# Kernel tuning notes

Measured on AMD Instinct MI355X. Metric: run time of the kernel, lower is better.

The kernel has to match this reference:

```python
import jax, jax.numpy as jnp
import numpy as np

NUM_HEADS = 4
GROUPS = 8          # min(8, ch) with ch=256
EPS = 1e-5          # torch GroupNorm default eps


def setup_inputs() -> dict:
    key = jax.random.key(0)
    ks = jax.random.split(key, 3)
    b, c, h, w = 8, 256, 32, 32
    x = jax.random.normal(ks[0], (b, c, h, w), jnp.float32)
    gn_gamma = jnp.ones((c,), jnp.float32)
    gn_beta = jnp.zeros((c,), jnp.float32)
    qkv_w = jax.random.normal(ks[1], (3 * c, c), jnp.float32) * (c ** -0.5)
    qkv_b = jnp.zeros((3 * c,), jnp.float32)
    proj_w = jax.random.normal(ks[2], (c, c), jnp.float32) * (c ** -0.5)
    proj_b = jnp.zeros((c,), jnp.float32)
    return {"x": x, "gn_gamma": gn_gamma, "gn_beta": gn_beta,
            "qkv_w": qkv_w, "qkv_b": qkv_b, "proj_w": proj_w, "proj_b": proj_b}


def _group_norm(x, gamma, beta):
    b, c, h, w = x.shape
    xg = x.reshape(b, GROUPS, c // GROUPS, h, w)
    mean = xg.mean(axis=(2, 3, 4), keepdims=True)
    var = xg.var(axis=(2, 3, 4), keepdims=True)
    xn = ((xg - mean) * jax.lax.rsqrt(var + EPS)).reshape(b, c, h, w)
    return xn * gamma[None, :, None, None] + beta[None, :, None, None]


def reference(x, gn_gamma, gn_beta, qkv_w, qkv_b, proj_w, proj_b):
    b, c, h, w = x.shape
    dh = c // NUM_HEADS
    xn = _group_norm(x, gn_gamma, gn_beta)
    # 1x1 conv == channel matmul
    qkv = jnp.einsum('oc,bchw->bohw', qkv_w, xn) + qkv_b[None, :, None, None]
    qkv = qkv.reshape(b, 3, NUM_HEADS, dh, h * w)
    q, k, v = qkv[:, 0], qkv[:, 1], qkv[:, 2]   # each (b, n, dh, hw)
    scale = dh ** -0.5
    # full (hw x hw) attention matrix, matching the original explicit einsum
    attn = jax.nn.softmax(jnp.einsum('bncd,bnce->bnde', q, k) * scale, axis=-1)
    out = jnp.einsum('bnde,bnce->bncd', attn, v).reshape(b, c, h, w)
    out = jnp.einsum('oc,bchw->bohw', proj_w, out) + proj_b[None, :, None, None]
    return x + out
```

## Files before the change

### kernel.cpp

```cpp
#include <hip/hip_runtime.h>
#include <stdint.h>

typedef __attribute__((ext_vector_type(8))) short short8;
typedef __attribute__((ext_vector_type(4))) float f32x4;

#define BB 8
#define CC 256
#define PP 1024
#define NH 4
#define DH 64

__device__ __forceinline__ unsigned short f2bf(float f) {
  union { float f; unsigned u; } v; v.f = f;
  unsigned r = v.u + 0x7FFFu + ((v.u >> 16) & 1u);
  return (unsigned short)(r >> 16);
}

__device__ __forceinline__ f32x4 mfma16(short8 a, short8 b, f32x4 c) {
  return __builtin_amdgcn_mfma_f32_16x16x32_bf16(a, b, c, 0, 0, 0);
}

__global__ __launch_bounds__(256) void prep(
    const float* __restrict__ x, float2* __restrict__ part,
    const float* __restrict__ qkvw, const float* __restrict__ projw,
    unsigned short* __restrict__ wall) {
  int blk = blockIdx.x;
  int tid = threadIdx.x;
  if (blk < 512) {
    int sl = blk & 7, g = (blk >> 3) & 7, b = blk >> 6;
    const float4* xb =
        (const float4*)(x + (size_t)(b * CC + g * 32) * PP) + sl * 1024;
    float s = 0.f, q = 0.f;
    for (int i = tid; i < 1024; i += 256) {
      float4 v = xb[i];
      s += v.x + v.y + v.z + v.w;
      q += v.x * v.x + v.y * v.y + v.z * v.z + v.w * v.w;
    }
    for (int off = 32; off > 0; off >>= 1) {
      s += __shfl_down(s, off);
      q += __shfl_down(q, off);
    }
    __shared__ float rs[4], rq[4];
    int w = tid >> 6;
    if ((tid & 63) == 0) { rs[w] = s; rq[w] = q; }
    __syncthreads();
    if (tid == 0)
      part[blk] = make_float2(rs[0] + rs[1] + rs[2] + rs[3],
                              rq[0] + rq[1] + rq[2] + rq[3]);
  } else {
    int i4 = (blk - 512) * 256 + tid;
    float4 v = (i4 < 49152) ? ((const float4*)qkvw)[i4]
                            : ((const float4*)projw)[i4 - 49152];
    ushort4 o;
    o.x = f2bf(v.x); o.y = f2bf(v.y); o.z = f2bf(v.z); o.w = f2bf(v.w);
    ((ushort4*)wall)[i4] = o;
  }
}

__global__ __launch_bounds__(256) void norm_t(
    const float* __restrict__ x, const float2* __restrict__ part,
    const float* __restrict__ gamma, const float* __restrict__ beta,
    unsigned short* __restrict__ xnT) {
  int p0 = blockIdx.x * 64, c0 = blockIdx.y * 64, b = blockIdx.z;
  int tid = threadIdx.x;
  __shared__ float ms[2], rstd[2];
  __shared__ unsigned short T[64][72];
  if (tid < 2) {
    int g = blockIdx.y * 2 + tid;
    float S = 0.f, Q = 0.f;
    for (int i = 0; i < 8; ++i) {
      float2 pp = part[b * 64 + g * 8 + i];
      S += pp.x; Q += pp.y;
    }
    float mean = S * (1.f / 32768.f);
    float var = Q * (1.f / 32768.f) - mean * mean;
    ms[tid] = mean;
    rstd[tid] = rsqrtf(var + 1e-5f);
  }
  __syncthreads();
  for (int it = 0; it < 4; ++it) {
    int l = tid + 256 * it;
    int cc = l >> 4, p4 = l & 15;
    int c = c0 + cc, gi = cc >> 5;
    float sc = rstd[gi] * gamma[c];
    float sh = beta[c] - ms[gi] * sc;
    float4 v = *(const float4*)(x + (size_t)(b * CC + c) * PP + p0 + p4 * 4);
    T[p4 * 4 + 0][cc] = f2bf(v.x * sc + sh);
    T[p4 * 4 + 1][cc] = f2bf(v.y * sc + sh);
    T[p4 * 4 + 2][cc] = f2bf(v.z * sc + sh);
    T[p4 * 4 + 3][cc] = f2bf(v.w * sc + sh);
  }
  __syncthreads();
  for (int it = 0; it < 2; ++it) {
    int l = tid + 256 * it;
    int p = l >> 3, seg = l & 7;
    *(short8*)(xnT + ((size_t)b * PP + p0 + p) * CC + c0 + seg * 8) =
        *(const short8*)&T[p][seg * 8];
  }
}

__global__ __launch_bounds__(256) void qkv_gemm(
    const unsigned short* __restrict__ xnT, const unsigned short* __restrict__ wbf,
    const float* __restrict__ qkvb, unsigned short* __restrict__ qb,
    unsigned short* __restrict__ kb, unsigned short* __restrict__ vT) {
  int p0 = blockIdx.x * 128, o0 = blockIdx.y * 128, b = blockIdx.z;
  int tid = threadIdx.x;
  int w = tid >> 6, lane = tid & 63, lq = lane >> 4, ln = lane & 15;
  int wy = w >> 1, wx = w & 1;
  __shared__ unsigned short A_l[128][40];
  __shared__ unsigned short B_l[128][40];
  f32x4 acc[4][4];
  for (int i = 0; i < 4; ++i)
    for (int j = 0; j < 4; ++j) acc[i][j] = (f32x4){0.f, 0.f, 0.f, 0.f};
  for (int kc = 0; kc < 256; kc += 32) {
    for (int it = 0; it < 2; ++it) {
      int l = tid + 256 * it;
      int row = l >> 2, seg = l & 3;
      *(short8*)&A_l[row][seg * 8] =
          *(const short8*)(xnT + ((size_t)b * PP + p0 + row) * CC + kc + seg * 8);
      *(short8*)&B_l[row][seg * 8] =
          *(const short8*)(wbf + (size_t)(o0 + row) * CC + kc + seg * 8);
    }
    __syncthreads();
    short8 af[4], bf[4];
    for (int i = 0; i < 4; ++i)
      af[i] = *(const short8*)&A_l[wy * 64 + i * 16 + ln][lq * 8];
    for (int j = 0; j < 4; ++j)
      bf[j] = *(const short8*)&B_l[wx * 64 + j * 16 + ln][lq * 8];
    for (int i = 0; i < 4; ++i)
      for (int j = 0; j < 4; ++j) acc[i][j] = mfma16(af[i], bf[j], acc[i][j]);
    __syncthreads();
  }
  for (int i = 0; i < 4; ++i) {
    for (int j = 0; j < 4; ++j) {
      int o = o0 + wx * 64 + j * 16 + ln;
      int s = o >> 8, h = (o >> 6) & 3, ch = o & 63;
      float bias = qkvb[o];
      float mul = (s == 0) ? 0.125f : 1.0f;
      size_t bh = (size_t)b * NH + h;
      for (int r = 0; r < 4; ++r) {
        int p = p0 + wy * 64 + i * 16 + lq * 4 + r;
        unsigned short val = f2bf((acc[i][j][r] + bias) * mul);
        if (s == 2) {
          vT[(bh * DH + ch) * PP + p] = val;
        } else {
          unsigned short* dst = (s == 0) ? qb : kb;
          dst[(bh * PP + p) * DH + ch] = val;
        }
      }
    }
  }
}

__global__ __launch_bounds__(256) void attn(
    const unsigned short* __restrict__ qb, const unsigned short* __restrict__ kb,
    const unsigned short* __restrict__ vT, unsigned short* __restrict__ attnT) {
  int d0 = blockIdx.x * 64, h = blockIdx.y, b = blockIdx.z;
  int tid = threadIdx.x;
  int w = tid >> 6, lane = tid & 63, lq = lane >> 4, ln = lane & 15;
  size_t bh = (size_t)b * NH + h;
  const unsigned short* qbase = qb + bh * PP * DH;
  const unsigned short* kbase = kb + bh * PP * DH;
  const unsigned short* vbase = vT + bh * DH * PP;
  __shared__ unsigned short K_l[128][72];
  __shared__ unsigned short V_l[64][136];
  __shared__ unsigned short P_l[64][140];
  unsigned short (*O_l)[72] = (unsigned short (*)[72]) & P_l[0][0];

  int ke = tid >> 1, kseg = tid & 1;
  int vch = tid >> 2, vseg = tid & 3;

  short8 qf[2];
  {
    int d = d0 + w * 16 + ln;
    qf[0] = *(const short8*)(qbase + (size_t)d * DH + lq * 8);
    qf[1] = *(const short8*)(qbase + (size_t)d * DH + 32 + lq * 8);
  }
  float l_sum = 0.f;
  f32x4 o_acc[4];
  for (int i = 0; i < 4; ++i) o_acc[i] = (f32x4){0.f, 0.f, 0.f, 0.f};

  short8 kr[4], vr[4];
#pragma unroll
  for (int i = 0; i < 4; ++i)
    kr[i] = *(const short8*)(kbase + (size_t)ke * DH + kseg * 32 + i * 8);
#pragma unroll
  for (int i = 0; i < 4; ++i)
    vr[i] = *(const short8*)(vbase + (size_t)vch * PP + vseg * 32 + i * 8);

  for (int e0 = 0; e0 < PP; e0 += 128) {
#pragma unroll
    for (int i = 0; i < 4; ++i)
      *(short8*)&K_l[ke][kseg * 32 + i * 8] = kr[i];
#pragma unroll
    for (int i = 0; i < 4; ++i)
      *(short8*)&V_l[vch][vseg * 32 + i * 8] = vr[i];
    if (e0 + 128 < PP) {
      int en = e0 + 128;
#pragma unroll
      for (int i = 0; i < 4; ++i)
        kr[i] = *(const short8*)(kbase + (size_t)(en + ke) * DH + kseg * 32 + i * 8);
#pragma unroll
      for (int i = 0; i < 4; ++i)
        vr[i] = *(const short8*)(vbase + (size_t)vch * PP + en + vseg * 32 + i * 8);
    }
    __syncthreads();
    f32x4 sc[8];
#pragma unroll
    for (int ns = 0; ns < 8; ++ns) {
      f32x4 a = (f32x4){0.f, 0.f, 0.f, 0.f};
      a = mfma16(*(const short8*)&K_l[ns * 16 + ln][lq * 8], qf[0], a);
      a = mfma16(*(const short8*)&K_l[ns * 16 + ln][32 + lq * 8], qf[1], a);
      sc[ns] = a;
    }
#pragma unroll
    for (int ns = 0; ns < 8; ++ns) {
      float p0 = __expf(fminf(sc[ns][0], 60.f));
      float p1 = __expf(fminf(sc[ns][1], 60.f));
      float p2 = __expf(fminf(sc[ns][2], 60.f));
      float p3 = __expf(fminf(sc[ns][3], 60.f));
      l_sum += (p0 + p1) + (p2 + p3);
      union { unsigned short u[4]; unsigned long long ll; } pk;
      pk.u[0] = f2bf(p0); pk.u[1] = f2bf(p1);
      pk.u[2] = f2bf(p2); pk.u[3] = f2bf(p3);
      *(unsigned long long*)&P_l[w * 16 + ln][ns * 16 + lq * 4] = pk.ll;
    }
#pragma unroll
    for (int t = 0; t < 4; ++t) {
      short8 pb = *(const short8*)&P_l[w * 16 + ln][t * 32 + lq * 8];
#pragma unroll
      for (int cs = 0; cs < 4; ++cs)
        o_acc[cs] = mfma16(
            *(const short8*)&V_l[cs * 16 + ln][t * 32 + lq * 8], pb, o_acc[cs]);
    }
    __syncthreads();
  }
  float rsum = l_sum;
  rsum += __shfl_xor(rsum, 16);
  rsum += __shfl_xor(rsum, 32);
  float inv = 1.f / rsum;
#pragma unroll
  for (int cs = 0; cs < 4; ++cs) {
    union { unsigned short u[4]; unsigned long long ll; } pk;
#pragma unroll
    for (int r = 0; r < 4; ++r) pk.u[r] = f2bf(o_acc[cs][r] * inv);
    *(unsigned long long*)&O_l[w * 16 + ln][cs * 16 + lq * 4] = pk.ll;
  }
  __syncthreads();
  for (int it = 0; it < 2; ++it) {
    int l = tid + 256 * it;
    int dd = l >> 3, seg = l & 7;
    *(short8*)(attnT + ((size_t)b * PP + d0 + dd) * CC + h * DH + seg * 8) =
        *(const short8*)&O_l[dd][seg * 8];
  }
}

__global__ __launch_bounds__(256) void proj_gemm(
    const unsigned short* __restrict__ attnT, const unsigned short* __restrict__ pwbf,
    const float* __restrict__ projb, const float* __restrict__ x,
    float* __restrict__ out) {
  int p0 = blockIdx.x * 128, o0 = blockIdx.y * 64, b = blockIdx.z;
  int tid = threadIdx.x;
  int w = tid >> 6, lane = tid & 63, lq = lane >> 4, ln = lane & 15;
  __shared__ unsigned short A_l[64][40];
  __shared__ unsigned short B_l[128][40];
  f32x4 acc[4][2];
  for (int i = 0; i < 4; ++i)
    for (int j = 0; j < 2; ++j) acc[i][j] = (f32x4){0.f, 0.f, 0.f, 0.f};
  for (int kc = 0; kc < 256; kc += 32) {
    {
      int row = tid >> 2, seg = tid & 3;
      *(short8*)&A_l[row][seg * 8] =
          *(const short8*)(pwbf + (size_t)(o0 + row) * CC + kc + seg * 8);
    }
    for (int it = 0; it < 2; ++it) {
      int l = tid + 256 * it;
      int row = l >> 2, seg = l & 3;
      *(short8*)&B_l[row][seg * 8] =
          *(const short8*)(attnT + ((size_t)b * PP + p0 + row) * CC + kc + seg * 8);
    }
    __syncthreads();
    short8 af[4], bfr[2];
    for (int i = 0; i < 4; ++i)
      af[i] = *(const short8*)&A_l[i * 16 + ln][lq * 8];
    for (int j = 0; j < 2; ++j)
      bfr[j] = *(const short8*)&B_l[w * 32 + j * 16 + ln][lq * 8];
    for (int i = 0; i < 4; ++i)
      for (int j = 0; j < 2; ++j) acc[i][j] = mfma16(af[i], bfr[j], acc[i][j]);
    __syncthreads();
  }
  for (int i = 0; i < 4; ++i) {
    for (int j = 0; j < 2; ++j) {
      int p = p0 + w * 32 + j * 16 + ln;
      for (int r = 0; r < 4; ++r) {
        int o = o0 + i * 16 + lq * 4 + r;
        size_t idx = ((size_t)b * CC + o) * PP + p;
        out[idx] = x[idx] + projb[o] + acc[i][j][r];
      }
    }
  }
}

extern "C" void kernel_launch(void* const* d_in, const int* in_sizes, int n_in,
                              void* d_out, int out_size, void* d_ws, size_t ws_size,
                              hipStream_t stream) {
  const float* x = (const float*)d_in[0];
  const float* gamma = (const float*)d_in[1];
  const float* beta = (const float*)d_in[2];
  const float* qkvw = (const float*)d_in[3];
  const float* qkvb = (const float*)d_in[4];
  const float* projw = (const float*)d_in[5];
  const float* projb = (const float*)d_in[6];
  float* out = (float*)d_out;
  char* ws = (char*)d_ws;

  float2* part = (float2*)(ws + 0);
  unsigned short* xnT = (unsigned short*)(ws + 16384);
  unsigned short* wall = (unsigned short*)(ws + 4210688);
  unsigned short* pwbf = wall + 768 * 256;
  unsigned short* qb = (unsigned short*)(ws + 4734976);
  unsigned short* kb = (unsigned short*)(ws + 8929280);
  unsigned short* vT = (unsigned short*)(ws + 13123584);
  unsigned short* attnT = (unsigned short*)(ws + 17317888);

  prep<<<768, 256, 0, stream>>>(x, part, qkvw, projw, wall);
  norm_t<<<dim3(16, 4, 8), 256, 0, stream>>>(x, part, gamma, beta, xnT);
  qkv_gemm<<<dim3(8, 6, 8), 256, 0, stream>>>(xnT, wall, qkvb, qb, kb, vT);
  attn<<<dim3(16, 4, 8), 256, 0, stream>>>(qb, kb, vT, attnT);
  proj_gemm<<<dim3(8, 4, 8), 256, 0, stream>>>(attnT, pwbf, projb, x, out);
}
```

Measured before the change: 123.0 us.

## Fuse GroupNorm into QKV GEMM, use exp2 softmax, vectorize V stores

New measurement: 119.7 us. -2.7%, faster.

```diff
diff --git a/kernel.cpp b/kernel.cpp
--- a/kernel.cpp
+++ b/kernel.cpp
@@ -9,6 +9,8 @@
 #define PP 1024
 #define NH 4
 #define DH 64
+
+#define QSCALE 0.18033688f
 
 __device__ __forceinline__ unsigned short f2bf(float f) {
   union { float f; unsigned u; } v; v.f = f;
@@ -57,78 +59,71 @@
   }
 }
 
-__global__ __launch_bounds__(256) void norm_t(
+__global__ __launch_bounds__(256) void nqkv(
     const float* __restrict__ x, const float2* __restrict__ part,
     const float* __restrict__ gamma, const float* __restrict__ beta,
-    unsigned short* __restrict__ xnT) {
-  int p0 = blockIdx.x * 64, c0 = blockIdx.y * 64, b = blockIdx.z;
-  int tid = threadIdx.x;
-  __shared__ float ms[2], rstd[2];
-  __shared__ unsigned short T[64][72];
-  if (tid < 2) {
-    int g = blockIdx.y * 2 + tid;
-    float S = 0.f, Q = 0.f;
-    for (int i = 0; i < 8; ++i) {
-      float2 pp = part[b * 64 + g * 8 + i];
-      S += pp.x; Q += pp.y;
-    }
-    float mean = S * (1.f / 32768.f);
-    float var = Q * (1.f / 32768.f) - mean * mean;
-    ms[tid] = mean;
-    rstd[tid] = rsqrtf(var + 1e-5f);
-  }
-  __syncthreads();
-  for (int it = 0; it < 4; ++it) {
-    int l = tid + 256 * it;
-    int cc = l >> 4, p4 = l & 15;
-    int c = c0 + cc, gi = cc >> 5;
-    float sc = rstd[gi] * gamma[c];
-    float sh = beta[c] - ms[gi] * sc;
-    float4 v = *(const float4*)(x + (size_t)(b * CC + c) * PP + p0 + p4 * 4);
-    T[p4 * 4 + 0][cc] = f2bf(v.x * sc + sh);
-    T[p4 * 4 + 1][cc] = f2bf(v.y * sc + sh);
-    T[p4 * 4 + 2][cc] = f2bf(v.z * sc + sh);
-    T[p4 * 4 + 3][cc] = f2bf(v.w * sc + sh);
-  }
-  __syncthreads();
-  for (int it = 0; it < 2; ++it) {
-    int l = tid + 256 * it;
-    int p = l >> 3, seg = l & 7;
-    *(short8*)(xnT + ((size_t)b * PP + p0 + p) * CC + c0 + seg * 8) =
-        *(const short8*)&T[p][seg * 8];
-  }
-}
-
-__global__ __launch_bounds__(256) void qkv_gemm(
-    const unsigned short* __restrict__ xnT, const unsigned short* __restrict__ wbf,
-    const float* __restrict__ qkvb, unsigned short* __restrict__ qb,
-    unsigned short* __restrict__ kb, unsigned short* __restrict__ vT) {
+    const unsigned short* __restrict__ wbf, const float* __restrict__ qkvb,
+    unsigned short* __restrict__ qb, unsigned short* __restrict__ kb,
+    unsigned short* __restrict__ vT) {
   int p0 = blockIdx.x * 128, o0 = blockIdx.y * 128, b = blockIdx.z;
   int tid = threadIdx.x;
   int w = tid >> 6, lane = tid & 63, lq = lane >> 4, ln = lane & 15;
   int wy = w >> 1, wx = w & 1;
   __shared__ unsigned short A_l[128][40];
   __shared__ unsigned short B_l[128][40];
+  __shared__ float scs[256], shs[256];
+  __shared__ float g_m[8], g_r[8];
+  if (tid < 8) {
+    float S = 0.f, Q = 0.f;
+    for (int i = 0; i < 8; ++i) {
+      float2 pp = part[b * 64 + tid * 8 + i];
+      S += pp.x; Q += pp.y;
+    }
+    float mean = S * (1.f / 32768.f);
+    float var = Q * (1.f / 32768.f) - mean * mean;
+    g_m[tid] = mean;
+    g_r[tid] = rsqrtf(var + 1e-5f);
+  }
+  __syncthreads();
+  {
+    int c = tid;
+    float sc = g_r[c >> 5] * gamma[c];
+    scs[c] = sc;
+    shs[c] = beta[c] - g_m[c >> 5] * sc;
+  }
+  __syncthreads();
   f32x4 acc[4][4];
   for (int i = 0; i < 4; ++i)
     for (int j = 0; j < 4; ++j) acc[i][j] = (f32x4){0.f, 0.f, 0.f, 0.f};
+  int cc = tid >> 3, ps = tid & 7;
   for (int kc = 0; kc < 256; kc += 32) {
+    {
+      float sc = scs[kc + cc], sh = shs[kc + cc];
+      const float* xr = x + ((size_t)(b * CC + kc + cc)) * PP + p0;
+#pragma unroll
+      for (int i = 0; i < 4; ++i) {
+        int p = ps * 4 + 32 * i;
+        float4 v = *(const float4*)(xr + p);
+        A_l[p + 0][cc] = f2bf(v.x * sc + sh);
+        A_l[p + 1][cc] = f2bf(v.y * sc + sh);
+        A_l[p + 2][cc] = f2bf(v.z * sc + sh);
+        A_l[p + 3][cc] = f2bf(v.w * sc + sh);
+      }
+    }
     for (int it = 0; it < 2; ++it) {
       int l = tid + 256 * it;
       int row = l >> 2, seg = l & 3;
-      *(short8*)&A_l[row][seg * 8] =
-          *(const short8*)(xnT + ((size_t)b * PP + p0 + row) * CC + kc + seg * 8);
       *(short8*)&B_l[row][seg * 8] =
           *(const short8*)(wbf + (size_t)(o0 + row) * CC + kc + seg * 8);
     }
     __syncthreads();
-    short8 af[4], bf[4];
+    short8 af[4], bfr[4];
     for (int i = 0; i < 4; ++i)
       af[i] = *(const short8*)&A_l[wy * 64 + i * 16 + ln][lq * 8];
     for (int j = 0; j < 4; ++j)
-      bf[j] = *(const short8*)&B_l[wx * 64 + j * 16 + ln][lq * 8];
-    for (int i = 0; i < 4; ++i)
-      for (int j = 0; j < 4; ++j) acc[i][j] = mfma16(af[i], bf[j], acc[i][j]);
+      bfr[j] = *(const short8*)&B_l[wx * 64 + j * 16 + ln][lq * 8];
+    for (int i = 0; i < 4; ++i)
+      for (int j = 0; j < 4; ++j) acc[i][j] = mfma16(af[i], bfr[j], acc[i][j]);
     __syncthreads();
   }
   for (int i = 0; i < 4; ++i) {
@@ -136,17 +131,20 @@
       int o = o0 + wx * 64 + j * 16 + ln;
       int s = o >> 8, h = (o >> 6) & 3, ch = o & 63;
       float bias = qkvb[o];
-      float mul = (s == 0) ? 0.125f : 1.0f;
+      float mul = (s == 0) ? QSCALE : 1.0f;
       size_t bh = (size_t)b * NH + h;
-      for (int r = 0; r < 4; ++r) {
-        int p = p0 + wy * 64 + i * 16 + lq * 4 + r;
-        unsigned short val = f2bf((acc[i][j][r] + bias) * mul);
-        if (s == 2) {
-          vT[(bh * DH + ch) * PP + p] = val;
-        } else {
-          unsigned short* dst = (s == 0) ? qb : kb;
-          dst[(bh * PP + p) * DH + ch] = val;
-        }
+      int pbase = p0 + wy * 64 + i * 16 + lq * 4;
+      if (s == 2) {
+        union { unsigned short u[4]; unsigned long long ll; } pk;
+#pragma unroll
+        for (int r = 0; r < 4; ++r) pk.u[r] = f2bf(acc[i][j][r] + bias);
+        *(unsigned long long*)(vT + (bh * DH + ch) * PP + pbase) = pk.ll;
+      } else {
+        unsigned short* dst = (s == 0) ? qb : kb;
+#pragma unroll
+        for (int r = 0; r < 4; ++r)
+          dst[(bh * PP + pbase + r) * DH + ch] =
+              f2bf((acc[i][j][r] + bias) * mul);
       }
     }
   }
@@ -215,10 +213,10 @@
     }
 #pragma unroll
     for (int ns = 0; ns < 8; ++ns) {
-      float p0 = __expf(fminf(sc[ns][0], 60.f));
-      float p1 = __expf(fminf(sc[ns][1], 60.f));
-      float p2 = __expf(fminf(sc[ns][2], 60.f));
-      float p3 = __expf(fminf(sc[ns][3], 60.f));
+      float p0 = __builtin_amdgcn_exp2f(fminf(sc[ns][0], 86.f));
+      float p1 = __builtin_amdgcn_exp2f(fminf(sc[ns][1], 86.f));
+      float p2 = __builtin_amdgcn_exp2f(fminf(sc[ns][2], 86.f));
+      float p3 = __builtin_amdgcn_exp2f(fminf(sc[ns][3], 86.f));
       l_sum += (p0 + p1) + (p2 + p3);
       union { unsigned short u[4]; unsigned long long ll; } pk;
       pk.u[0] = f2bf(p0); pk.u[1] = f2bf(p1);
@@ -315,7 +313,6 @@
   char* ws = (char*)d_ws;
 
   float2* part = (float2*)(ws + 0);
-  unsigned short* xnT = (unsigned short*)(ws + 16384);
   unsigned short* wall = (unsigned short*)(ws + 4210688);
   unsigned short* pwbf = wall + 768 * 256;
   unsigned short* qb = (unsigned short*)(ws + 4734976);
@@ -324,8 +321,8 @@
   unsigned short* attnT = (unsigned short*)(ws + 17317888);
 
   prep<<<768, 256, 0, stream>>>(x, part, qkvw, projw, wall);
-  norm_t<<<dim3(16, 4, 8), 256, 0, stream>>>(x, part, gamma, beta, xnT);
-  qkv_gemm<<<dim3(8, 6, 8), 256, 0, stream>>>(xnT, wall, qkvb, qb, kb, vT);
+  nqkv<<<dim3(8, 6, 8), 256, 0, stream>>>(x, part, gamma, beta, wall, qkvb,
+                                          qb, kb, vT);
   attn<<<dim3(16, 4, 8), 256, 0, stream>>>(qb, kb, vT, attnT);
   proj_gemm<<<dim3(8, 4, 8), 256, 0, stream>>>(attnT, pwbf, projb, x, out);
 }
```
